# Optimization experiments

Measured on AMD Instinct MI355X. Metric: run time of the kernel, lower is better.

Reference implementation:

```python
import jax, jax.numpy as jnp
import numpy as np

D_MODEL = 2048
MAX_SEQ_LEN = 8192
LN_EPS = 1e-5


def _generate_spine(max_len):
    s = [0, 2, 4]
    while True:
        nxt = 2 * s[-1] + 2 * s[-2] + 2 * s[-3]
        if nxt >= max_len:
            break
        s.append(nxt)
    return np.asarray(s, dtype=np.int32)


def setup_inputs() -> dict:
    key = jax.random.key(0)
    k_x, k_w = jax.random.split(key)
    B, S, D = 2, MAX_SEQ_LEN, D_MODEL
    x = jax.random.normal(k_x, (B, S, D), dtype=jnp.float32)
    # torch nn.Linear(2D -> D): weight [D, 2D], kaiming-uniform-ish init
    lim = 1.0 / np.sqrt(2 * D)
    gate_w = jax.random.uniform(k_w, (D, 2 * D), dtype=jnp.float32, minval=-lim, maxval=lim)
    gate_b = jnp.zeros((D,), dtype=jnp.float32)
    ln_g = jnp.ones((D,), dtype=jnp.float32)
    ln_b = jnp.zeros((D,), dtype=jnp.float32)
    spine = jnp.asarray(_generate_spine(MAX_SEQ_LEN))  # indices < S
    return {"x": x, "gate_w": gate_w, "gate_b": gate_b,
            "ln_g": ln_g, "ln_b": ln_b, "spine": spine}


def reference(x, gate_w, gate_b, ln_g, ln_b, spine):
    # All spine positions are distinct and each update depends only on the
    # original row at that position, so the python loop in the torch module
    # fuses into one batched gather -> gate -> layernorm -> scatter.
    h = x[:, spine, :] * 0.5                         # [B, K, D]  (h_lattice == h_attention)
    combined = jnp.concatenate([h, h], axis=-1)      # [B, K, 2D]
    g = jax.nn.sigmoid(jnp.einsum('bkf,df->bkd', combined, gate_w) + gate_b)
    x_out = g * h + (1.0 - g) * h                    # == h, kept for fidelity
    mean = jnp.mean(x_out, axis=-1, keepdims=True)
    var = jnp.var(x_out, axis=-1, keepdims=True)
    update = (x_out - mean) * jax.lax.rsqrt(var + LN_EPS) * ln_g + ln_b
    return x.at[:, spine, :].set(update)
```

## Files before the change

kernel.cpp:

```cpp
#include <hip/hip_runtime.h>


#define D_MODEL 2048
#define SEQ_LEN 8192
#define LN_EPS 1e-5f

typedef float f32x4 __attribute__((ext_vector_type(4)));

__global__ __launch_bounds__(256) void copy_kernel(const f32x4* __restrict__ in,
                                                   f32x4* __restrict__ out,
                                                   long n4) {
    long i = (long)blockIdx.x * blockDim.x + threadIdx.x;
    long stride = (long)gridDim.x * blockDim.x;
    for (; i < n4; i += stride) {
        f32x4 v = __builtin_nontemporal_load(&in[i]);
        __builtin_nontemporal_store(v, &out[i]);
    }
}

__global__ __launch_bounds__(256) void spine_ln_kernel(const float* __restrict__ x,
                                                       const float* __restrict__ ln_g,
                                                       const float* __restrict__ ln_b,
                                                       const int* __restrict__ spine,
                                                       float* __restrict__ out,
                                                       int K) {
    const int bk = blockIdx.x;
    const int b = bk / K;
    const int k = bk - b * K;
    const long row_base = (long)b * ((long)SEQ_LEN * D_MODEL)
                        + (long)spine[k] * D_MODEL;

    const int t = threadIdx.x;
    const float4* xin = (const float4*)(x + row_base);

    float4 h[2];
    float sum = 0.f, ss = 0.f;
#pragma unroll
    for (int j = 0; j < 2; ++j) {
        float4 v = xin[t * 2 + j];
        v.x *= 0.5f; v.y *= 0.5f; v.z *= 0.5f; v.w *= 0.5f;
        h[j] = v;
        sum += v.x + v.y + v.z + v.w;
        ss  += v.x * v.x + v.y * v.y + v.z * v.z + v.w * v.w;
    }

#pragma unroll
    for (int off = 32; off > 0; off >>= 1) {
        sum += __shfl_down(sum, off, 64);
        ss  += __shfl_down(ss,  off, 64);
    }
    __shared__ float s_sum[4];
    __shared__ float s_ss[4];
    const int wave = t >> 6;
    const int lane = t & 63;
    if (lane == 0) { s_sum[wave] = sum; s_ss[wave] = ss; }
    __syncthreads();
    if (t == 0) {
        float S = 0.f, Q = 0.f;
#pragma unroll
        for (int w = 0; w < 4; ++w) { S += s_sum[w]; Q += s_ss[w]; }
        const float mean = S * (1.0f / (float)D_MODEL);
        const float var  = Q * (1.0f / (float)D_MODEL) - mean * mean;
        s_sum[0] = mean;
        s_ss[0]  = rsqrtf(var + LN_EPS);
    }
    __syncthreads();
    const float mean = s_sum[0];
    const float inv  = s_ss[0];

    float4* o4 = (float4*)(out + row_base);
    const float4* g4 = (const float4*)ln_g;
    const float4* b4 = (const float4*)ln_b;
#pragma unroll
    for (int j = 0; j < 2; ++j) {
        const float4 g  = g4[t * 2 + j];
        const float4 bb = b4[t * 2 + j];
        float4 v = h[j];
        float4 r;
        r.x = (v.x - mean) * inv * g.x + bb.x;
        r.y = (v.y - mean) * inv * g.y + bb.y;
        r.z = (v.z - mean) * inv * g.z + bb.z;
        r.w = (v.w - mean) * inv * g.w + bb.w;
        o4[t * 2 + j] = r;
    }
}

extern "C" void kernel_launch(void* const* d_in, const int* in_sizes, int n_in,
                              void* d_out, int out_size, void* d_ws, size_t ws_size,
                              hipStream_t stream) {
    const float* x    = (const float*)d_in[0];
    const float* ln_g = (const float*)d_in[3];
    const float* ln_b = (const float*)d_in[4];
    const int*  spine = (const int*)d_in[5];
    float* out = (float*)d_out;

    const long n  = (long)in_sizes[0];
    const long n4 = n >> 2;
    const int  K  = in_sizes[5];
    const int  B  = (int)(n / ((long)SEQ_LEN * D_MODEL));

    copy_kernel<<<2048, 256, 0, stream>>>((const f32x4*)x, (f32x4*)out, n4);

    spine_ln_kernel<<<B * K, 256, 0, stream>>>(x, ln_g, ln_b, spine, out, K);
}
```

Baseline: 249.5 us.

## Fuse bulk copy and spine layernorm into one row-per-block kernel

Replaces the separate grid-stride copy kernel and the spine layernorm kernel with a single kernel that launches one block per row. Each block scans the spine list to decide whether to copy its row unchanged or to compute the layernorm update. This removes a second launch and avoids writing spine rows twice, but it launches 16384 small blocks, each moving only 8KB and each doing a serial scan of the spine array.

```diff
diff --git a/kernel.cpp b/kernel.cpp
--- a/kernel.cpp
+++ b/kernel.cpp
@@ -7,38 +7,39 @@
 
 typedef float f32x4 __attribute__((ext_vector_type(4)));
 
-__global__ __launch_bounds__(256) void copy_kernel(const f32x4* __restrict__ in,
-                                                   f32x4* __restrict__ out,
-                                                   long n4) {
-    long i = (long)blockIdx.x * blockDim.x + threadIdx.x;
-    long stride = (long)gridDim.x * blockDim.x;
-    for (; i < n4; i += stride) {
-        f32x4 v = __builtin_nontemporal_load(&in[i]);
-        __builtin_nontemporal_store(v, &out[i]);
-    }
-}
+__global__ __launch_bounds__(256) void fused_copy_ln_kernel(
+        const float* __restrict__ x,
+        const float* __restrict__ ln_g,
+        const float* __restrict__ ln_b,
+        const int* __restrict__ spine,
+        float* __restrict__ out,
+        int K) {
+    const long r = blockIdx.x;
+    const long base = r * D_MODEL;
+    const int  s = (int)(r & (SEQ_LEN - 1));
 
-__global__ __launch_bounds__(256) void spine_ln_kernel(const float* __restrict__ x,
-                                                       const float* __restrict__ ln_g,
-                                                       const float* __restrict__ ln_b,
-                                                       const int* __restrict__ spine,
-                                                       float* __restrict__ out,
-                                                       int K) {
-    const int bk = blockIdx.x;
-    const int b = bk / K;
-    const int k = bk - b * K;
-    const long row_base = (long)b * ((long)SEQ_LEN * D_MODEL)
-                        + (long)spine[k] * D_MODEL;
+    bool is_spine = false;
+    for (int k = 0; k < K; ++k) is_spine |= (spine[k] == s);
 
     const int t = threadIdx.x;
-    const float4* xin = (const float4*)(x + row_base);
+    const f32x4* in4 = (const f32x4*)(x + base);
+    f32x4* o4 = (f32x4*)(out + base);
 
-    float4 h[2];
+    if (!is_spine) {
+#pragma unroll
+        for (int j = 0; j < 2; ++j) {
+            f32x4 v = __builtin_nontemporal_load(&in4[j * 256 + t]);
+            __builtin_nontemporal_store(v, &o4[j * 256 + t]);
+        }
+        return;
+    }
+
+    f32x4 h[2];
     float sum = 0.f, ss = 0.f;
 #pragma unroll
     for (int j = 0; j < 2; ++j) {
-        float4 v = xin[t * 2 + j];
-        v.x *= 0.5f; v.y *= 0.5f; v.z *= 0.5f; v.w *= 0.5f;
+        f32x4 v = in4[j * 256 + t];
+        v *= 0.5f;
         h[j] = v;
         sum += v.x + v.y + v.z + v.w;
         ss  += v.x * v.x + v.y * v.y + v.z * v.z + v.w * v.w;
@@ -68,20 +69,19 @@
     const float mean = s_sum[0];
     const float inv  = s_ss[0];
 
-    float4* o4 = (float4*)(out + row_base);
-    const float4* g4 = (const float4*)ln_g;
-    const float4* b4 = (const float4*)ln_b;
+    const f32x4* g4 = (const f32x4*)ln_g;
+    const f32x4* b4 = (const f32x4*)ln_b;
 #pragma unroll
     for (int j = 0; j < 2; ++j) {
-        const float4 g  = g4[t * 2 + j];
-        const float4 bb = b4[t * 2 + j];
-        float4 v = h[j];
-        float4 r;
-        r.x = (v.x - mean) * inv * g.x + bb.x;
-        r.y = (v.y - mean) * inv * g.y + bb.y;
-        r.z = (v.z - mean) * inv * g.z + bb.z;
-        r.w = (v.w - mean) * inv * g.w + bb.w;
-        o4[t * 2 + j] = r;
+        const f32x4 g  = g4[j * 256 + t];
+        const f32x4 bb = b4[j * 256 + t];
+        f32x4 v = h[j];
+        f32x4 rr;
+        rr.x = (v.x - mean) * inv * g.x + bb.x;
+        rr.y = (v.y - mean) * inv * g.y + bb.y;
+        rr.z = (v.z - mean) * inv * g.z + bb.z;
+        rr.w = (v.w - mean) * inv * g.w + bb.w;
+        o4[j * 256 + t] = rr;
     }
 }
 
@@ -94,12 +94,9 @@
     const int*  spine = (const int*)d_in[5];
     float* out = (float*)d_out;
 
-    const long n  = (long)in_sizes[0];
-    const long n4 = n >> 2;
-    const int  K  = in_sizes[5];
-    const int  B  = (int)(n / ((long)SEQ_LEN * D_MODEL));
+    const long n     = (long)in_sizes[0];
+    const int  K     = in_sizes[5];
+    const long nrows = n / D_MODEL;
 
-    copy_kernel<<<2048, 256, 0, stream>>>((const f32x4*)x, (f32x4*)out, n4);
-
-    spine_ln_kernel<<<B * K, 256, 0, stream>>>(x, ln_g, ln_b, spine, out, K);
+    fused_copy_ln_kernel<<<(int)nrows, 256, 0, stream>>>(x, ln_g, ln_b, spine, out, K);
 }
```

Measured after the change: 246.4 us. About the same (-1.3%).
